# Optimization experiments

Hardware: AMD Instinct MI355X
Metric: run time of the kernel (lower is better)

Reference implementation:

```python
import jax, jax.numpy as jnp
import numpy as np

# model config (see init_kwargs)
L, H, NH, KVH, DH, I, P, F, T = 8, 1024, 16, 2, 64, 4096, 4, 64, 10
QLEN = 9                      # 1 dit token + P cond tokens + P latent tokens
GROUPS = NH // KVH            # GQA repeat factor
PREFIX = P + 1                # prefix_plus
SCALE = DH ** -0.25           # folded into rope cos/sin (applied to q AND k)


def setup_inputs() -> dict:
    key = jax.random.key(0)
    ks = jax.random.split(key, 16)
    g = lambda i, shape, s=0.02: jax.random.normal(ks[i], shape, jnp.float32) * s
    # sway-sampled timestep schedule -> dt table (matches torch precompute)
    ts = np.linspace(1.0, 0.0, T + 1, dtype=np.float32)
    ts = (ts + 1.0 * (np.cos(np.pi / 2 * ts) - 1.0 + ts))[1:]
    dt_all = jnp.asarray((ts[:-1] - ts[1:]).reshape(1, 1, T - 1))
    # rope tables with attention scale folded in
    pos = np.arange(QLEN, dtype=np.float32)
    inv_freq = 1.0 / (10000.0 ** (np.arange(0, DH, 2, dtype=np.float32) / DH))
    freqs = np.concatenate([np.outer(pos, inv_freq)] * 2, axis=-1)  # [QLEN, DH]
    cos_q = jnp.asarray(np.cos(freqs)[None, None] * SCALE)  # [1,1,QLEN,DH]
    sin_q = jnp.asarray(np.sin(freqs)[None, None] * SCALE)
    return dict(
        random=g(0, (1, P, F), 1.0),
        dit_hidden=g(1, (1, 1, H), 1.0),
        feat_cond=g(2, (2, P, H), 1.0),
        cfg_value=jnp.full((1,), 2.5, jnp.float32),
        cfg_value_minus=jnp.full((1,), -1.5, jnp.float32),
        t_all=g(3, (1, T - 1, H), 1.0),   # precomputed time_mlp output table
        dt_all=dt_all, cos_q=cos_q, sin_q=sin_q,
        W_in=g(4, (F, H)), b_in=jnp.zeros((H,), jnp.float32),
        ln1_w=jnp.ones((L, H), jnp.float32),
        Wq=g(5, (L, H, NH * DH)), Wk=g(6, (L, H, KVH * DH)),
        Wv=g(7, (L, H, KVH * DH)), Wo=g(8, (L, NH * DH, H)),
        ln2_w=jnp.ones((L, H), jnp.float32),
        Wg=g(9, (L, H, I)), Wu=g(10, (L, H, I)), Wd=g(11, (L, I, H)),
        norm_w=jnp.ones((H,), jnp.float32),
        W_out=g(12, (H, F)), b_out=jnp.zeros((F,), jnp.float32),
        step=jnp.zeros((1,), jnp.int32),
    )


def _rms(x, w, eps=1e-6):
    return x * jax.lax.rsqrt(jnp.mean(x * x, axis=-1, keepdims=True) + eps) * w


def _rot_half(x):
    x1, x2 = jnp.split(x, 2, axis=-1)
    return jnp.concatenate([-x2, x1], axis=-1)


def reference(random, dit_hidden, feat_cond, cfg_value, cfg_value_minus,
              t_all, dt_all, cos_q, sin_q, W_in, b_in, ln1_w, Wq, Wk, Wv, Wo,
              ln2_w, Wg, Wu, Wd, norm_w, W_out, b_out, step):
    t = t_all[:, step]                                   # [1,1,H]
    dt = dt_all[..., step]                               # [1,1,1]
    dh = jnp.concatenate([dit_hidden + t, t], axis=0)    # CFG doubling -> [2,1,H]
    x = random @ W_in + b_in                             # [1,P,H]
    h = jnp.concatenate([dh, feat_cond, jnp.concatenate([x, x], axis=0)], axis=1)  # [2,QLEN,H]

    def layer(h, p):
        ln1, wq, wk, wv, wo, ln2, wg, wu, wd = p
        hn = _rms(h, ln1)
        q = (hn @ wq).reshape(2, QLEN, NH, DH).transpose(0, 2, 1, 3)
        k = (hn @ wk).reshape(2, QLEN, KVH, DH).transpose(0, 2, 1, 3)
        v = (hn @ wv).reshape(2, QLEN, KVH, DH).transpose(0, 2, 1, 3)
        # rope with head_dim**-0.25 scale folded into cos/sin (applied to q and k)
        q = q * cos_q + _rot_half(q) * sin_q
        k = k * cos_q + _rot_half(k) * sin_q
        k = jnp.repeat(k, GROUPS, axis=1)                # repeat_k (GQA)
        v = jnp.repeat(v, GROUPS, axis=1)                # repeat_v
        attn = jax.nn.softmax(jnp.einsum('bhqd,bhkd->bhqk', q, k), axis=-1)
        out = jnp.einsum('bhqk,bhkd->bhqd', attn, v)
        out = out.transpose(0, 2, 1, 3).reshape(2, QLEN, NH * DH)
        h = h + out @ wo
        hn2 = _rms(h, ln2)
        h = h + (jax.nn.silu(hn2 @ wg) * (hn2 @ wu)) @ wd
        return h, None

    h, _ = jax.lax.scan(layer, h, (ln1_w, Wq, Wk, Wv, Wo, ln2_w, Wg, Wu, Wd))
    h = _rms(h[:, PREFIX:], norm_w)                      # drop prefix -> [2,P,H]
    out = h @ W_out + b_out                              # [2,P,F]
    pos, neg = out[0:1], out[1:2]
    pf = pos.reshape(1, 1, -1)                           # [1,1,P*F]
    nf = neg.reshape(1, -1, 1)                           # [1,P*F,1]
    st = (pf @ nf) / (jnp.swapaxes(nf, 1, 2) @ nf + 1e-7)  # rescaled CFG, [1,1,1]
    dphi = cfg_value_minus * neg * st + cfg_value * pos
    next_random = random - dt * dphi
    return step + 1, next_random
```

## Files before the change

### kernel.cpp

```cpp
#include <hip/hip_runtime.h>

#define TOKENS 18
#define QLEN 9
#define HDIM 1024
#define IDIM 4096
#define NLAYER 8

#define HA_OFF    0u
#define HB_OFF    18432u
#define SQA_OFF   36864u
#define SQB_OFF   36936u
#define QKVR_OFF  37008u
#define QKVP_OFF  60048u
#define OPP_OFF   428688u
#define GUP_OFF   1018512u
#define M_OFF     3377808u
#define WDP_OFF   3451536u
#define OUTP_OFF  4631184u
#define TOTAL_F   4647568u

__device__ __forceinline__ void loadf2(float2* buf, const float* wp, int base, int stride) {
#pragma unroll
  for (int j = 0; j < 8; j++)
    buf[j] = *reinterpret_cast<const float2*>(wp + (size_t)(base + j) * stride);
}
__device__ __forceinline__ void fmaf2(float2* acc, const float2* buf,
                                      const float (*sb)[TOKENS], int base) {
#pragma unroll
  for (int j = 0; j < 8; j++) {
#pragma unroll
    for (int t = 0; t < TOKENS; t++) {
      float bv = sb[base + j][t];
      acc[t].x += bv * buf[j].x; acc[t].y += bv * buf[j].y;
    }
  }
}

__global__ __launch_bounds__(256) void k_embed(
    const float* __restrict__ rnd, const float* __restrict__ dit,
    const float* __restrict__ feat, const float* __restrict__ t_all,
    const float* __restrict__ W_in, const float* __restrict__ b_in,
    const int* __restrict__ step, float* __restrict__ ws) {
  int t = blockIdx.x >> 2, q4 = blockIdx.x & 3, c0 = q4 * 256;
  int b = t / QLEN, q = t - b * QLEN;
  int tid = threadIdx.x, c = c0 + tid;
  int st = step[0];
  __shared__ float rl[64];
  __shared__ float pr[4];
  float v;
  if (q == 0) {
    v = t_all[(size_t)st * HDIM + c] + (b == 0 ? dit[c] : 0.f);
  } else if (q <= 4) {
    v = feat[(size_t)(b * 4 + q - 1) * HDIM + c];
  } else {
    int p = q - 5;
    if (tid < 64) rl[tid] = rnd[p * 64 + tid];
    __syncthreads();
    float a = b_in[c];
#pragma unroll 8
    for (int f = 0; f < 64; f++) a += rl[f] * W_in[(size_t)f * HDIM + c];
    v = a;
  }
  ws[HA_OFF + (size_t)t * HDIM + c] = v;
  float sq = v * v;
#pragma unroll
  for (int off = 32; off >= 1; off >>= 1) sq += __shfl_down(sq, off);
  if ((tid & 63) == 0) pr[tid >> 6] = sq;
  __syncthreads();
  if (tid == 0) ws[SQA_OFF + (size_t)t * 4 + q4] = pr[0] + pr[1] + pr[2] + pr[3];
}

__global__ __launch_bounds__(256) void k_qkv(
    const float* __restrict__ Wq, const float* __restrict__ Wk,
    const float* __restrict__ Wv, const float* __restrict__ ln1,
    float* __restrict__ ws, int layer) {
  int bx = blockIdx.x, ks = blockIdx.y, r0 = ks * 64, tid = threadIdx.x;
  __shared__ float s_b[64][TOKENS];
  __shared__ float s_rstd[TOKENS];
  float W[64];
  const float* wp;
  int stride;
  int col = 0;
  if (bx < 4) {
    col = bx * 256 + tid;
    wp = Wq + ((size_t)layer << 20) + (size_t)r0 * HDIM + col;
    stride = HDIM;
  } else {
    wp = (tid < 128)
       ? (Wk + (size_t)layer * 131072 + (size_t)r0 * 128 + tid)
       : (Wv + (size_t)layer * 131072 + (size_t)r0 * 128 + (tid - 128));
    stride = 128;
  }
#pragma unroll
  for (int j = 0; j < 64; j++) W[j] = wp[(size_t)j * stride];
  if (tid < TOKENS) {
    float s = ws[SQA_OFF + tid * 4] + ws[SQA_OFF + tid * 4 + 1]
            + ws[SQA_OFF + tid * 4 + 2] + ws[SQA_OFF + tid * 4 + 3];
    s_rstd[tid] = rsqrtf(s * (1.f / HDIM) + 1e-6f);
  }
  const float* lw = ln1 + (size_t)layer * HDIM;
  for (int i = tid; i < 64 * TOKENS; i += 256) {
    int t = i % TOKENS, r = i / TOKENS;
    s_b[r][t] = ws[HA_OFF + (size_t)t * HDIM + r0 + r] * lw[r0 + r];
  }
  __syncthreads();
  float acc[TOKENS];
#pragma unroll
  for (int t = 0; t < TOKENS; t++) acc[t] = 0.f;
#pragma unroll
  for (int j = 0; j < 64; j++) {
#pragma unroll
    for (int t = 0; t < TOKENS; t++) acc[t] += s_b[j][t] * W[j];
  }
  float* qp = ws + QKVP_OFF + (size_t)ks * (TOKENS * 1280);
  if (bx < 4) {
#pragma unroll
    for (int t = 0; t < TOKENS; t++) qp[(size_t)t * 1280 + col] = acc[t] * s_rstd[t];
  } else {
#pragma unroll
    for (int t = 0; t < TOKENS; t++) qp[(size_t)t * 1280 + 1024 + tid] = acc[t] * s_rstd[t];
  }
}

__global__ __launch_bounds__(256) void k_redq(float* __restrict__ ws) {
  int el = blockIdx.x * 256 + threadIdx.x;
  float s = 0.f;
#pragma unroll 8
  for (int p = 0; p < 16; p++) s += ws[QKVP_OFF + (size_t)p * (TOKENS * 1280) + el];
  ws[QKVR_OFF + el] = s;
}

__global__ __launch_bounds__(256) void k_wo(
    const float* __restrict__ Wo, const float* __restrict__ cosq,
    const float* __restrict__ sinq, float* __restrict__ ws, int layer) {
  const float* qkv = ws + QKVR_OFF;
  int bx = blockIdx.x, by = blockIdx.y, tid = threadIdx.x;
  int r0 = by * 32, head = r0 >> 6, kvh = head >> 3, d0 = r0 & 63;
  __shared__ float lq[2][QLEN][68];
  __shared__ float lk[2][QLEN][68];
  __shared__ float lv[2][QLEN][33];
  __shared__ float sP[2][QLEN][12];
  __shared__ float sA[32][TOKENS];
  for (int i = tid; i < 2 * QLEN * 64; i += 256) {
    int d = i & 63, qi = (i >> 6) % QLEN, b = i / (QLEN * 64);
    const float* qr = qkv + (size_t)(b * QLEN + qi) * 1280;
    float c = cosq[qi * 64 + d], s = sinq[qi * 64 + d];
    float qv = qr[head * 64 + d];
    float qo = (d < 32) ? -qr[head * 64 + d + 32] : qr[head * 64 + d - 32];
    lq[b][qi][d] = qv * c + qo * s;
    float kv = qr[1024 + kvh * 64 + d];
    float ko = (d < 32) ? -qr[1024 + kvh * 64 + d + 32] : qr[1024 + kvh * 64 + d - 32];
    lk[b][qi][d] = kv * c + ko * s;
  }
  for (int i = tid; i < 2 * QLEN * 32; i += 256) {
    int d = i & 31, ki = (i >> 5) % QLEN, b = i / (QLEN * 32);
    lv[b][ki][d] = qkv[(size_t)(b * QLEN + ki) * 1280 + 1152 + kvh * 64 + d0 + d];
  }
  __syncthreads();
  for (int i = tid; i < 2 * QLEN * QLEN; i += 256) {
    int ki = i % QLEN, qi = (i / QLEN) % QLEN, b = i / (QLEN * QLEN);
    float s = 0.f;
#pragma unroll
    for (int d = 0; d < 64; d++) s += lq[b][qi][d] * lk[b][ki][d];
    sP[b][qi][ki] = s;
  }
  __syncthreads();
  if (tid < TOKENS) {
    int b = tid / QLEN, qi = tid % QLEN;
    float m = -1e30f;
#pragma unroll
    for (int k = 0; k < QLEN; k++) m = fmaxf(m, sP[b][qi][k]);
    float e[QLEN], sum = 0.f;
#pragma unroll
    for (int k = 0; k < QLEN; k++) { e[k] = expf(sP[b][qi][k] - m); sum += e[k]; }
    float inv = 1.f / sum;
#pragma unroll
    for (int k = 0; k < QLEN; k++) sP[b][qi][k] = e[k] * inv;
  }
  __syncthreads();
  for (int i = tid; i < 32 * TOKENS; i += 256) {
    int dd = i / TOKENS, t = i - dd * TOKENS;
    int b = t / QLEN, qi = t % QLEN;
    float a = 0.f;
#pragma unroll
    for (int k = 0; k < QLEN; k++) a += sP[b][qi][k] * lv[b][k][dd];
    sA[dd][t] = a;
  }
  __syncthreads();
  int col = bx * 512 + tid * 2;
  const float* wp = Wo + ((size_t)layer << 20) + (size_t)r0 * HDIM + col;
  float2 A[8], B[8];
  float2 acc[TOKENS];
#pragma unroll
  for (int t = 0; t < TOKENS; t++) acc[t] = make_float2(0.f, 0.f);
  loadf2(A, wp, 0, HDIM); loadf2(B, wp, 8, HDIM);
  fmaf2(acc, A, sA, 0);   loadf2(A, wp, 16, HDIM);
  fmaf2(acc, B, sA, 8);   loadf2(B, wp, 24, HDIM);
  fmaf2(acc, A, sA, 16);  fmaf2(acc, B, sA, 24);
  float* op = ws + OPP_OFF + (size_t)by * (TOKENS * HDIM);
#pragma unroll
  for (int t = 0; t < TOKENS; t++)
    *reinterpret_cast<float2*>(op + (size_t)t * HDIM + col) = acc[t];
}

__global__ __launch_bounds__(256) void k_redo(float* __restrict__ ws) {
  int t = blockIdx.x >> 2, q4 = blockIdx.x & 3;
  int tid = threadIdx.x, c = q4 * 256 + tid;
  __shared__ float pr[4];
  float v = ws[HA_OFF + (size_t)t * HDIM + c];
  const float* pp = ws + OPP_OFF + (size_t)t * HDIM + c;
#pragma unroll 8
  for (int p = 0; p < 32; p++) v += pp[(size_t)p * (TOKENS * HDIM)];
  ws[HB_OFF + (size_t)t * HDIM + c] = v;
  float sq = v * v;
#pragma unroll
  for (int off = 32; off >= 1; off >>= 1) sq += __shfl_down(sq, off);
  if ((tid & 63) == 0) pr[tid >> 6] = sq;
  __syncthreads();
  if (tid == 0) ws[SQB_OFF + (size_t)t * 4 + q4] = pr[0] + pr[1] + pr[2] + pr[3];
}

__global__ __launch_bounds__(256) void k_gu(
    const float* __restrict__ Wg, const float* __restrict__ Wu,
    const float* __restrict__ ln2, float* __restrict__ ws, int layer) {
  int cs = blockIdx.x, ks = blockIdx.y, r0 = ks * 64, tid = threadIdx.x;
  __shared__ float s_b[TOKENS][64];
  __shared__ float s_rstd[TOKENS];
  int base = (cs & 15) * 256;
  const float* W = (cs < 16 ? Wg : Wu) + ((size_t)layer << 22);
  const float* wp = W + (size_t)r0 * IDIM + base + tid;
  float wbuf[64];
#pragma unroll
  for (int j = 0; j < 64; j++) wbuf[j] = wp[(size_t)j * IDIM];
  if (tid < TOKENS) {
    float s = ws[SQB_OFF + tid * 4] + ws[SQB_OFF + tid * 4 + 1]
            + ws[SQB_OFF + tid * 4 + 2] + ws[SQB_OFF + tid * 4 + 3];
    s_rstd[tid] = rsqrtf(s * (1.f / HDIM) + 1e-6f);
  }
  const float* lw = ln2 + (size_t)layer * HDIM;
  for (int i = tid; i < TOKENS * 64; i += 256) {
    int t = i >> 6, r = i & 63;
    s_b[t][r] = ws[HB_OFF + (size_t)t * HDIM + r0 + r] * lw[r0 + r];
  }
  __syncthreads();
  float acc[TOKENS];
#pragma unroll
  for (int t = 0; t < TOKENS; t++) acc[t] = 0.f;
#pragma unroll
  for (int j = 0; j < 64; j++) {
#pragma unroll
    for (int t = 0; t < TOKENS; t++) acc[t] += s_b[t][j] * wbuf[j];
  }
  int outcol = (cs < 16 ? base : 4096 + base) + tid;
  float* gp = ws + GUP_OFF + (size_t)ks * (TOKENS * 8192) + outcol;
#pragma unroll
  for (int t = 0; t < TOKENS; t++) gp[(size_t)t * 8192] = acc[t] * s_rstd[t];
}

__global__ __launch_bounds__(256) void k_m(float* __restrict__ ws) {
  int el = blockIdx.x * 256 + threadIdx.x;
  int t = el >> 12, j = el & 4095;
  const float* gp = ws + GUP_OFF + (size_t)t * 8192 + j;
  float g = 0.f, u = 0.f;
#pragma unroll 8
  for (int p = 0; p < 16; p++) {
    g += gp[(size_t)p * (TOKENS * 8192)];
    u += gp[(size_t)p * (TOKENS * 8192) + 4096];
  }
  ws[M_OFF + (size_t)t * 4096 + j] = (g / (1.f + expf(-g))) * u;
}

__global__ __launch_bounds__(256) void k_wd(
    const float* __restrict__ Wd, float* __restrict__ ws, int layer) {
  int ks2 = blockIdx.x >> 3, cs = blockIdx.x & 7;
  int r0 = ks2 * 128, c0 = cs * 128;
  int tid = threadIdx.x, colt = tid & 127, hf = tid >> 7;
  __shared__ float s_b[TOKENS][128];
  for (int i = tid; i < TOKENS * 128; i += 256) {
    int t = i >> 7, r = i & 127;
    s_b[t][r] = ws[M_OFF + (size_t)t * 4096 + r0 + r];
  }
  __syncthreads();
  int col = c0 + colt;
  const float* wp = Wd + ((size_t)layer << 22) + (size_t)(r0 + hf * 64) * HDIM + col;
  float wbuf[64];
#pragma unroll
  for (int j = 0; j < 64; j++) wbuf[j] = wp[(size_t)j * HDIM];
  float acc[TOKENS];
#pragma unroll
  for (int t = 0; t < TOKENS; t++) acc[t] = 0.f;
#pragma unroll
  for (int j = 0; j < 64; j++) {
#pragma unroll
    for (int t = 0; t < TOKENS; t++) acc[t] += s_b[t][hf * 64 + j] * wbuf[j];
  }
  int slab = ks2 * 2 + hf;
  float* wdp = ws + WDP_OFF + (size_t)slab * (TOKENS * HDIM) + col;
#pragma unroll
  for (int t = 0; t < TOKENS; t++) wdp[(size_t)t * HDIM] = acc[t];
}

__global__ __launch_bounds__(256) void k_hup(float* __restrict__ ws) {
  int t = blockIdx.x >> 2, q4 = blockIdx.x & 3;
  int tid = threadIdx.x, c = q4 * 256 + tid;
  __shared__ float pr[4];
  float v = ws[HB_OFF + (size_t)t * HDIM + c];
  const float* pp = ws + WDP_OFF + (size_t)t * HDIM + c;
#pragma unroll 8
  for (int p = 0; p < 64; p++) v += pp[(size_t)p * (TOKENS * HDIM)];
  ws[HA_OFF + (size_t)t * HDIM + c] = v;
  float sq = v * v;
#pragma unroll
  for (int off = 32; off >= 1; off >>= 1) sq += __shfl_down(sq, off);
  if ((tid & 63) == 0) pr[tid >> 6] = sq;
  __syncthreads();
  if (tid == 0) ws[SQA_OFF + (size_t)t * 4 + q4] = pr[0] + pr[1] + pr[2] + pr[3];
}

__global__ __launch_bounds__(256) void k_out(
    const float* __restrict__ Wout, const float* __restrict__ normw,
    float* __restrict__ ws) {
  const float* h = ws + HA_OFF;
  float* outp = ws + OUTP_OFF;
  __shared__ float s_rstd[8];
  __shared__ float s_b[128][8];
  int tid = threadIdx.x;
  if (tid < 8) {
    int tix = (tid >> 2) * QLEN + 5 + (tid & 3);
    float s = ws[SQA_OFF + tix * 4] + ws[SQA_OFF + tix * 4 + 1]
            + ws[SQA_OFF + tix * 4 + 2] + ws[SQA_OFF + tix * 4 + 3];
    s_rstd[tid] = rsqrtf(s * (1.f / HDIM) + 1e-6f);
  }
  __syncthreads();
  int r0 = blockIdx.x * 128;
  for (int i = tid; i < 128 * 8; i += 256) {
    int r = i >> 3, s = i & 7;
    int tix = (s >> 2) * QLEN + 5 + (s & 3);
    s_b[r][s] = h[(size_t)tix * HDIM + r0 + r] * normw[r0 + r] * s_rstd[s];
  }
  __syncthreads();
  int colc = tid & 63, rsub = tid >> 6;
  const float* wp = Wout + (size_t)(r0 + rsub * 32) * 64 + colc;
  float acc[8];
#pragma unroll
  for (int s = 0; s < 8; s++) acc[s] = 0.f;
#pragma unroll 8
  for (int r = 0; r < 32; r++) {
    float w = wp[(size_t)r * 64];
#pragma unroll
    for (int s = 0; s < 8; s++) acc[s] += s_b[rsub * 32 + r][s] * w;
  }
  float* slot = outp + (size_t)(blockIdx.x * 4 + rsub) * 512;
#pragma unroll
  for (int s = 0; s < 8; s++) slot[s * 64 + colc] = acc[s];
}

__global__ __launch_bounds__(256) void k_final(
    const float* __restrict__ rnd, const float* __restrict__ cfg,
    const float* __restrict__ cfgm, const float* __restrict__ dt_all,
    const float* __restrict__ bout, const int* __restrict__ step,
    const float* __restrict__ ws, float* __restrict__ out) {
  const float* outp = ws + OUTP_OFF;
  int tid = threadIdx.x;
  int f = tid & 63;
  float p = bout[f], n = bout[f];
#pragma unroll 8
  for (int pp = 0; pp < 32; pp++) {
    p += outp[(size_t)pp * 512 + tid];
    n += outp[(size_t)pp * 512 + 256 + tid];
  }
  float pn = p * n, nn = n * n;
#pragma unroll
  for (int off = 32; off >= 1; off >>= 1) {
    pn += __shfl_down(pn, off);
    nn += __shfl_down(nn, off);
  }
  __shared__ float red[8];
  __shared__ float s_st;
  int wave = tid >> 6, lane = tid & 63;
  if (lane == 0) { red[wave] = pn; red[4 + wave] = nn; }
  __syncthreads();
  if (tid == 0) {
    float PN = red[0] + red[1] + red[2] + red[3];
    float NN = red[4] + red[5] + red[6] + red[7];
    s_st = PN / (NN + 1e-7f);
  }
  __syncthreads();
  int st = step[0];
  float dphi = cfgm[0] * n * s_st + cfg[0] * p;
  float next = rnd[tid] - dt_all[st] * dphi;
  if (tid == 0) out[0] = (float)(st + 1);
  out[1 + tid] = next;
}

extern "C" void kernel_launch(void* const* d_in, const int* in_sizes, int n_in,
                              void* d_out, int out_size, void* d_ws, size_t ws_size,
                              hipStream_t stream) {
  const float* rnd   = (const float*)d_in[0];
  const float* dit   = (const float*)d_in[1];
  const float* feat  = (const float*)d_in[2];
  const float* cfg   = (const float*)d_in[3];
  const float* cfgm  = (const float*)d_in[4];
  const float* t_all = (const float*)d_in[5];
  const float* dt_al = (const float*)d_in[6];
  const float* cosq  = (const float*)d_in[7];
  const float* sinq  = (const float*)d_in[8];
  const float* W_in  = (const float*)d_in[9];
  const float* b_in  = (const float*)d_in[10];
  const float* ln1   = (const float*)d_in[11];
  const float* Wq    = (const float*)d_in[12];
  const float* Wk    = (const float*)d_in[13];
  const float* Wv    = (const float*)d_in[14];
  const float* Wo    = (const float*)d_in[15];
  const float* ln2   = (const float*)d_in[16];
  const float* Wg    = (const float*)d_in[17];
  const float* Wu    = (const float*)d_in[18];
  const float* Wd    = (const float*)d_in[19];
  const float* normw = (const float*)d_in[20];
  const float* Wout  = (const float*)d_in[21];
  const float* bout  = (const float*)d_in[22];
  const int*   step  = (const int*)d_in[23];
  float* ws = (float*)d_ws;

  k_embed<<<72, 256, 0, stream>>>(rnd, dit, feat, t_all, W_in, b_in, step, ws);
  for (int l = 0; l < NLAYER; l++) {
    k_qkv<<<dim3(5, 16), 256, 0, stream>>>(Wq, Wk, Wv, ln1, ws, l);
    k_redq<<<90, 256, 0, stream>>>(ws);
    k_wo<<<dim3(2, 32), 256, 0, stream>>>(Wo, cosq, sinq, ws, l);
    k_redo<<<72, 256, 0, stream>>>(ws);
    k_gu<<<dim3(32, 16), 256, 0, stream>>>(Wg, Wu, ln2, ws, l);
    k_m<<<288, 256, 0, stream>>>(ws);
    k_wd<<<256, 256, 0, stream>>>(Wd, ws, l);
    k_hup<<<72, 256, 0, stream>>>(ws);
  }
  k_out<<<8, 256, 0, stream>>>(Wout, normw, ws);
  k_final<<<1, 256, 0, stream>>>(rnd, cfg, cfgm, dt_al, bout, step, ws, (float*)d_out);
}
```

Baseline: 572.2 us.

## Fold reduction kernels into consumer GEMMs with atomic-flag inter-block sync

Removes the separate reduction launches (redq, redo, m, and hup for the inner layers) by having the first blocks of each consumer kernel do the split-K reduction. Each of those blocks then releases an atomic counter, and every block spins on it after prefetching its weight slice into registers. This halves the launches per layer and overlaps the weight loads with the reduction. It relies on all blocks being co-resident, since a spinning block can otherwise wait forever. It also needs a memset of the counters on every call.

New measurement: 1.094 ms. +91.2%, slower.

```diff
diff --git a/kernel.cpp b/kernel.cpp
--- a/kernel.cpp
+++ b/kernel.cpp
@@ -10,14 +10,24 @@
 #define HB_OFF    18432u
 #define SQA_OFF   36864u
 #define SQB_OFF   36936u
-#define QKVR_OFF  37008u
-#define QKVP_OFF  60048u
-#define OPP_OFF   428688u
-#define GUP_OFF   1018512u
-#define M_OFF     3377808u
-#define WDP_OFF   3451536u
-#define OUTP_OFF  4631184u
-#define TOTAL_F   4647568u
+#define CNT_OFF   37008u
+#define QKVR_OFF  37072u
+#define QKVP_OFF  60112u
+#define OPP_OFF   428752u
+#define GUP_OFF   1018576u
+#define M_OFF     3377872u
+#define WDP_OFF   3451600u
+#define OUTP_OFF  4631248u
+#define TOTAL_F   4647632u
+
+__device__ __forceinline__ void flag_release(unsigned* c) {
+  __threadfence();
+  __hip_atomic_fetch_add(c, 1u, __ATOMIC_RELEASE, __HIP_MEMORY_SCOPE_AGENT);
+}
+__device__ __forceinline__ void flag_spin(unsigned* c, unsigned tgt) {
+  while (__hip_atomic_load(c, __ATOMIC_ACQUIRE, __HIP_MEMORY_SCOPE_AGENT) < tgt)
+    __builtin_amdgcn_s_sleep(2);
+}
 
 __device__ __forceinline__ void loadf2(float2* buf, const float* wp, int base, int stride) {
 #pragma unroll
@@ -75,8 +85,28 @@
     const float* __restrict__ Wv, const float* __restrict__ ln1,
     float* __restrict__ ws, int layer) {
   int bx = blockIdx.x, ks = blockIdx.y, r0 = ks * 64, tid = threadIdx.x;
+  int id = ks * 5 + bx;
+  unsigned* cnt = (unsigned*)(ws + CNT_OFF) + layer;
   __shared__ float s_b[64][TOKENS];
   __shared__ float s_rstd[TOKENS];
+  __shared__ float pr[4];
+  if (layer > 0 && id < 72) {
+    int t = id >> 2, q4 = id & 3, c = q4 * 256 + tid;
+    float v = ws[HB_OFF + (size_t)t * HDIM + c];
+    const float* pp = ws + WDP_OFF + (size_t)t * HDIM + c;
+#pragma unroll 8
+    for (int p = 0; p < 64; p++) v += pp[(size_t)p * (TOKENS * HDIM)];
+    ws[HA_OFF + (size_t)t * HDIM + c] = v;
+    float sq = v * v;
+#pragma unroll
+    for (int off = 32; off >= 1; off >>= 1) sq += __shfl_down(sq, off);
+    if ((tid & 63) == 0) pr[tid >> 6] = sq;
+    __syncthreads();
+    if (tid == 0) {
+      ws[SQA_OFF + (size_t)t * 4 + q4] = pr[0] + pr[1] + pr[2] + pr[3];
+      flag_release(cnt);
+    }
+  }
   float W[64];
   const float* wp;
   int stride;
@@ -93,6 +123,10 @@
   }
 #pragma unroll
   for (int j = 0; j < 64; j++) W[j] = wp[(size_t)j * stride];
+  if (layer > 0) {
+    if (tid == 0) flag_spin(cnt, 72u);
+    __syncthreads();
+  }
   if (tid < TOKENS) {
     float s = ws[SQA_OFF + tid * 4] + ws[SQA_OFF + tid * 4 + 1]
             + ws[SQA_OFF + tid * 4 + 2] + ws[SQA_OFF + tid * 4 + 3];
@@ -122,19 +156,25 @@
   }
 }
 
-__global__ __launch_bounds__(256) void k_redq(float* __restrict__ ws) {
-  int el = blockIdx.x * 256 + threadIdx.x;
-  float s = 0.f;
-#pragma unroll 8
-  for (int p = 0; p < 16; p++) s += ws[QKVP_OFF + (size_t)p * (TOKENS * 1280) + el];
-  ws[QKVR_OFF + el] = s;
-}
-
 __global__ __launch_bounds__(256) void k_wo(
     const float* __restrict__ Wo, const float* __restrict__ cosq,
     const float* __restrict__ sinq, float* __restrict__ ws, int layer) {
+  int bid = blockIdx.x, tid = threadIdx.x;
+  unsigned* cnt = (unsigned*)(ws + CNT_OFF) + 8 + layer;
+  if (bid < 90) {
+    int el = bid * 256 + tid;
+    float s = 0.f;
+#pragma unroll 8
+    for (int p = 0; p < 16; p++) s += ws[QKVP_OFF + (size_t)p * (TOKENS * 1280) + el];
+    ws[QKVR_OFF + el] = s;
+    __syncthreads();
+    if (tid == 0) flag_release(cnt);
+  }
+  if (bid >= 64) return;
+  if (tid == 0) flag_spin(cnt, 90u);
+  __syncthreads();
   const float* qkv = ws + QKVR_OFF;
-  int bx = blockIdx.x, by = blockIdx.y, tid = threadIdx.x;
+  int bx = bid & 1, by = bid >> 1;
   int r0 = by * 32, head = r0 >> 6, kvh = head >> 3, d0 = r0 & 63;
   __shared__ float lq[2][QLEN][68];
   __shared__ float lk[2][QLEN][68];
@@ -203,35 +243,40 @@
     *reinterpret_cast<float2*>(op + (size_t)t * HDIM + col) = acc[t];
 }
 
-__global__ __launch_bounds__(256) void k_redo(float* __restrict__ ws) {
-  int t = blockIdx.x >> 2, q4 = blockIdx.x & 3;
-  int tid = threadIdx.x, c = q4 * 256 + tid;
-  __shared__ float pr[4];
-  float v = ws[HA_OFF + (size_t)t * HDIM + c];
-  const float* pp = ws + OPP_OFF + (size_t)t * HDIM + c;
-#pragma unroll 8
-  for (int p = 0; p < 32; p++) v += pp[(size_t)p * (TOKENS * HDIM)];
-  ws[HB_OFF + (size_t)t * HDIM + c] = v;
-  float sq = v * v;
-#pragma unroll
-  for (int off = 32; off >= 1; off >>= 1) sq += __shfl_down(sq, off);
-  if ((tid & 63) == 0) pr[tid >> 6] = sq;
-  __syncthreads();
-  if (tid == 0) ws[SQB_OFF + (size_t)t * 4 + q4] = pr[0] + pr[1] + pr[2] + pr[3];
-}
-
-__global__ __launch_bounds__(256) void k_gu(
+__global__ __launch_bounds__(256, 2) void k_gu(
     const float* __restrict__ Wg, const float* __restrict__ Wu,
     const float* __restrict__ ln2, float* __restrict__ ws, int layer) {
-  int cs = blockIdx.x, ks = blockIdx.y, r0 = ks * 64, tid = threadIdx.x;
+  int bid = blockIdx.x, tid = threadIdx.x;
+  int cs = bid >> 4, ks = bid & 15, r0 = ks * 64;
+  unsigned* cnt = (unsigned*)(ws + CNT_OFF) + 16 + layer;
   __shared__ float s_b[TOKENS][64];
   __shared__ float s_rstd[TOKENS];
+  __shared__ float pr[4];
+  if (bid < 72) {
+    int t = bid >> 2, q4 = bid & 3, c = q4 * 256 + tid;
+    float v = ws[HA_OFF + (size_t)t * HDIM + c];
+    const float* pp = ws + OPP_OFF + (size_t)t * HDIM + c;
+#pragma unroll 8
+    for (int p = 0; p < 32; p++) v += pp[(size_t)p * (TOKENS * HDIM)];
+    ws[HB_OFF + (size_t)t * HDIM + c] = v;
+    float sq = v * v;
+#pragma unroll
+    for (int off = 32; off >= 1; off >>= 1) sq += __shfl_down(sq, off);
+    if ((tid & 63) == 0) pr[tid >> 6] = sq;
+    __syncthreads();
+    if (tid == 0) {
+      ws[SQB_OFF + (size_t)t * 4 + q4] = pr[0] + pr[1] + pr[2] + pr[3];
+      flag_release(cnt);
+    }
+  }
   int base = (cs & 15) * 256;
   const float* W = (cs < 16 ? Wg : Wu) + ((size_t)layer << 22);
   const float* wp = W + (size_t)r0 * IDIM + base + tid;
   float wbuf[64];
 #pragma unroll
   for (int j = 0; j < 64; j++) wbuf[j] = wp[(size_t)j * IDIM];
+  if (tid == 0) flag_spin(cnt, 72u);
+  __syncthreads();
   if (tid < TOKENS) {
     float s = ws[SQB_OFF + tid * 4] + ws[SQB_OFF + tid * 4 + 1]
             + ws[SQB_OFF + tid * 4 + 2] + ws[SQB_OFF + tid * 4 + 3];
@@ -257,35 +302,41 @@
   for (int t = 0; t < TOKENS; t++) gp[(size_t)t * 8192] = acc[t] * s_rstd[t];
 }
 
-__global__ __launch_bounds__(256) void k_m(float* __restrict__ ws) {
-  int el = blockIdx.x * 256 + threadIdx.x;
-  int t = el >> 12, j = el & 4095;
-  const float* gp = ws + GUP_OFF + (size_t)t * 8192 + j;
-  float g = 0.f, u = 0.f;
-#pragma unroll 8
-  for (int p = 0; p < 16; p++) {
-    g += gp[(size_t)p * (TOKENS * 8192)];
-    u += gp[(size_t)p * (TOKENS * 8192) + 4096];
-  }
-  ws[M_OFF + (size_t)t * 4096 + j] = (g / (1.f + expf(-g))) * u;
-}
-
 __global__ __launch_bounds__(256) void k_wd(
     const float* __restrict__ Wd, float* __restrict__ ws, int layer) {
-  int ks2 = blockIdx.x >> 3, cs = blockIdx.x & 7;
+  int bid = blockIdx.x, tid = threadIdx.x;
+  unsigned* cnt = (unsigned*)(ws + CNT_OFF) + 24 + layer;
+  {
+    int el = bid * 256 + tid;
+    int t = el >> 12, j = el & 4095;
+    const float* gp = ws + GUP_OFF + (size_t)t * 8192 + j;
+    float g = 0.f, u = 0.f;
+#pragma unroll 8
+    for (int p = 0; p < 16; p++) {
+      g += gp[(size_t)p * (TOKENS * 8192)];
+      u += gp[(size_t)p * (TOKENS * 8192) + 4096];
+    }
+    ws[M_OFF + (size_t)t * 4096 + j] = (g / (1.f + expf(-g))) * u;
+    __syncthreads();
+    if (tid == 0) flag_release(cnt);
+  }
+  if (bid >= 256) return;
+  int ks2 = bid >> 3, cs = bid & 7;
   int r0 = ks2 * 128, c0 = cs * 128;
-  int tid = threadIdx.x, colt = tid & 127, hf = tid >> 7;
+  int colt = tid & 127, hf = tid >> 7;
   __shared__ float s_b[TOKENS][128];
+  int col = c0 + colt;
+  const float* wp = Wd + ((size_t)layer << 22) + (size_t)(r0 + hf * 64) * HDIM + col;
+  float wbuf[64];
+#pragma unroll
+  for (int j = 0; j < 64; j++) wbuf[j] = wp[(size_t)j * HDIM];
+  if (tid == 0) flag_spin(cnt, 288u);
+  __syncthreads();
   for (int i = tid; i < TOKENS * 128; i += 256) {
     int t = i >> 7, r = i & 127;
     s_b[t][r] = ws[M_OFF + (size_t)t * 4096 + r0 + r];
   }
   __syncthreads();
-  int col = c0 + colt;
-  const float* wp = Wd + ((size_t)layer << 22) + (size_t)(r0 + hf * 64) * HDIM + col;
-  float wbuf[64];
-#pragma unroll
-  for (int j = 0; j < 64; j++) wbuf[j] = wp[(size_t)j * HDIM];
   float acc[TOKENS];
 #pragma unroll
   for (int t = 0; t < TOKENS; t++) acc[t] = 0.f;
@@ -422,17 +473,16 @@
   const int*   step  = (const int*)d_in[23];
   float* ws = (float*)d_ws;
 
+  hipMemsetAsync((void*)(ws + CNT_OFF), 0, 64 * sizeof(unsigned), stream);
+
   k_embed<<<72, 256, 0, stream>>>(rnd, dit, feat, t_all, W_in, b_in, step, ws);
   for (int l = 0; l < NLAYER; l++) {
     k_qkv<<<dim3(5, 16), 256, 0, stream>>>(Wq, Wk, Wv, ln1, ws, l);
-    k_redq<<<90, 256, 0, stream>>>(ws);
-    k_wo<<<dim3(2, 32), 256, 0, stream>>>(Wo, cosq, sinq, ws, l);
-    k_redo<<<72, 256, 0, stream>>>(ws);
-    k_gu<<<dim3(32, 16), 256, 0, stream>>>(Wg, Wu, ln2, ws, l);
-    k_m<<<288, 256, 0, stream>>>(ws);
-    k_wd<<<256, 256, 0, stream>>>(Wd, ws, l);
-    k_hup<<<72, 256, 0, stream>>>(ws);
-  }
+    k_wo<<<96, 256, 0, stream>>>(Wo, cosq, sinq, ws, l);
+    k_gu<<<512, 256, 0, stream>>>(Wg, Wu, ln2, ws, l);
+    k_wd<<<288, 256, 0, stream>>>(Wd, ws, l);
+  }
+  k_hup<<<72, 256, 0, stream>>>(ws);
   k_out<<<8, 256, 0, stream>>>(Wout, normw, ws);
   k_final<<<1, 256, 0, stream>>>(rnd, cfg, cfgm, dt_al, bout, step, ws, (float*)d_out);
 }
```
